# Kernel tuning notes

Measured on AMD Instinct MI355X. Metric: run time of the kernel, lower is better.

## Reference

```python
import jax, jax.numpy as jnp
import numpy as np

COST_CLASS, COST_MASK, COST_DICE = 2.0, 5.0, 5.0
NUM_POINTS = 12544

def setup_inputs() -> dict:
    key = jax.random.key(0)
    k1, k2, k3, k4, k5 = jax.random.split(key, 5)
    bs, Q, K = 4, 100, 134
    H = W = 256
    M = 80
    P = H * W
    pred_logits = jax.random.normal(k1, (bs, Q, K), dtype=jnp.float32)
    pred_masks = jax.random.normal(k2, (bs, Q, H, W), dtype=jnp.float32)
    tgt_labels = jax.random.randint(k3, (M,), 0, K - 1, dtype=jnp.int32)
    # binary target masks, stored as float (matches .float() in torch code)
    tgt_masks = (jax.random.uniform(k4, (M, H, W)) > 0.5).astype(jnp.float32)
    # random subset of points without replacement (torch.randperm[:num_points])
    point_idx = jax.random.permutation(k5, P)[:NUM_POINTS].astype(jnp.int32)
    return {"pred_logits": pred_logits, "pred_masks": pred_masks,
            "tgt_labels": tgt_labels, "tgt_masks": tgt_masks,
            "point_idx": point_idx}

def reference(pred_logits, pred_masks, tgt_labels, tgt_masks, point_idx):
    bs, Q, K = pred_logits.shape
    N = bs * Q
    M = tgt_masks.shape[0]
    Pn = point_idx.shape[0]

    # class cost: -p[n, tgt_id[m]]
    out_prob = jax.nn.softmax(pred_logits.reshape(N, K), axis=-1)
    tgt_ids = jnp.clip(tgt_labels.astype(jnp.int32), 0, K - 1)
    cost_class = -out_prob[:, tgt_ids]                      # (N, M)

    # sampled mask logits / targets
    x = pred_masks.reshape(N, -1)[:, point_idx]             # (N, Pn) logits
    y = tgt_masks.reshape(M, -1)[:, point_idx]              # (M, Pn) binary float

    # BCE-with-logits cost, separable form:
    # mean_p[softplus(x) - x*y] = mean_p softplus(x) - (x @ y^T)/Pn
    sp_mean = jnp.mean(jax.nn.softplus(x), axis=-1)         # (N,)
    xy = jnp.einsum('np,mp->nm', x, y)                      # (N, M)
    cost_mask = sp_mean[:, None] - xy / Pn

    # dice cost
    s = jax.nn.sigmoid(x)                                   # (N, Pn)
    numer = 2.0 * jnp.einsum('np,mp->nm', s, y)             # (N, M)
    denom = jnp.sum(s, axis=-1)[:, None] + jnp.sum(y, axis=-1)[None, :]
    cost_dice = 1.0 - (numer + 1.0) / (denom + 1.0)

    C = COST_CLASS * cost_class + COST_MASK * cost_mask + COST_DICE * cost_dice
    return C.reshape(bs, Q, M)
```

## Files before the change

kernel.cpp:

```cpp
#include <hip/hip_runtime.h>
#include <math.h>

#define N_ROWS 400
#define M_ROWS 80
#define K_CLS  134
#define PN     12544
#define PFULL  65536
#define WORDS  (PFULL / 32)
#define NSUB   25
#define TSTEPS 392
#define TPB    2
#define KCG    49

#define GY_BLOCKS 245

#define CROWS  (N_ROWS + M_ROWS)
#define CHUNK  16384
#define CPB    (PFULL / CHUNK)

typedef __attribute__((ext_vector_type(4))) float  f32x4;
typedef __attribute__((ext_vector_type(8))) __bf16 bf16x8;

__device__ __forceinline__ float wave_reduce_sum(float v) {
#pragma unroll
    for (int off = 32; off > 0; off >>= 1) v += __shfl_down(v, off, 64);
    return v;
}

__global__ __launch_bounds__(1024) void sort_softmax_kernel(
        const int* __restrict__ point_idx,
        unsigned int* __restrict__ bitmap_g, int* __restrict__ rank_g,
        const float* __restrict__ pred_logits,
        float* __restrict__ rowmax, float* __restrict__ rowsum) {
    int tid = threadIdx.x;
    if (blockIdx.x == 0) {
        __shared__ unsigned int bits[WORDS];
        __shared__ int wtot[16], wbase[16];
        bits[tid] = 0u; bits[tid + 1024] = 0u;
        __syncthreads();
        for (int i = tid; i < PN; i += 1024) {
            int p = point_idx[i];
            atomicOr(&bits[p >> 5], 1u << (p & 31));
        }
        __syncthreads();
        unsigned int w0 = bits[tid * 2], w1 = bits[tid * 2 + 1];
        int cnt = __popc(w0) + __popc(w1);
        int lane = tid & 63, wid = tid >> 6;
        int v = cnt;
#pragma unroll
        for (int off = 1; off < 64; off <<= 1) {
            int u = __shfl_up(v, off, 64);
            if (lane >= off) v += u;
        }
        if (lane == 63) wtot[wid] = v;
        __syncthreads();
        if (tid == 0) {
            int run = 0;
#pragma unroll
            for (int i = 0; i < 16; ++i) { wbase[i] = run; run += wtot[i]; }
        }
        __syncthreads();
        int base = wbase[wid] + (v - cnt);
        bitmap_g[tid * 2]     = w0;
        bitmap_g[tid * 2 + 1] = w1;
        rank_g[tid * 2]       = base;
        rank_g[tid * 2 + 1]   = base + __popc(w0);
    } else {
        int wave = tid >> 6, lane = tid & 63;
        int n = (blockIdx.x - 1) * 16 + wave;
        const float* row = pred_logits + n * K_CLS;
        float mx = -1e30f;
        for (int k = lane; k < K_CLS; k += 64) mx = fmaxf(mx, row[k]);
#pragma unroll
        for (int off = 32; off > 0; off >>= 1) mx = fmaxf(mx, __shfl_down(mx, off, 64));
        mx = __shfl(mx, 0, 64);
        float se = 0.f;
        for (int k = lane; k < K_CLS; k += 64) se += expf(row[k] - mx);
        se = wave_reduce_sum(se);
        if (lane == 0) { rowmax[n] = mx; rowsum[n] = se; }
    }
}

__global__ __launch_bounds__(256) void compact_kernel(
        const float* __restrict__ pred_masks, const float* __restrict__ tgt_masks,
        const unsigned int* __restrict__ bitmap_g, const int* __restrict__ rank_g,
        float* __restrict__ Xc, float* __restrict__ Yc) {
    __shared__ unsigned int sb[CHUNK / 32];
    __shared__ int swb[CHUNK / 32];
    int b   = blockIdx.x;
    int row = b / CPB, ch = b % CPB;
    int tid = threadIdx.x;
    int w0  = ch * (CHUNK / 32);
    sb[tid]        = bitmap_g[w0 + tid];
    sb[tid + 256]  = bitmap_g[w0 + tid + 256];
    swb[tid]       = rank_g[w0 + tid];
    swb[tid + 256] = rank_g[w0 + tid + 256];
    __syncthreads();

    const float* src; float* dst;
    if (row < N_ROWS) {
        src = pred_masks + (size_t)row * PFULL;
        dst = Xc + (size_t)row * PN;
    } else {
        src = tgt_masks + (size_t)(row - N_ROWS) * PFULL;
        dst = Yc + (size_t)(row - N_ROWS) * PN;
    }
    int p0 = ch * CHUNK;
#pragma unroll
    for (int it = 0; it < CHUNK / (256 * 4); ++it) {
        int e = (it * 256 + tid) * 4;
        f32x4 v = *(const f32x4*)(src + p0 + e);
        unsigned int w = sb[e >> 5];
        int r = swb[e >> 5] + __popc(w & ((1u << (e & 31)) - 1u));
        unsigned int m4 = (w >> (e & 31)) & 0xFu;
        if (m4 & 1u) { dst[r++] = v[0]; }
        if (m4 & 2u) { dst[r++] = v[1]; }
        if (m4 & 4u) { dst[r++] = v[2]; }
        if (m4 & 8u) { dst[r]   = v[3]; }
    }
}

__global__ __launch_bounds__(512) void gather_y_kernel(
        const float* __restrict__ Yc,
        __bf16* __restrict__ Yb, float* __restrict__ ypart) {
    __shared__ float smem[128];
    int b = blockIdx.x;
    int j = b / 49, tch = b % 49;
    int wave = threadIdx.x >> 6, lane = threadIdx.x & 63;
    int colL = lane & 15, quad = lane >> 4;
    int m = 16 * j + colL;
    int t = tch * 8 + wave;
    int k0 = t * 32 + quad * 8;
    const float* yrow = Yc + (size_t)m * PN;
    f32x4 a = *(const f32x4*)(yrow + k0);
    f32x4 c = *(const f32x4*)(yrow + k0 + 4);
    bf16x8 v; float acc = 0.f;
#pragma unroll
    for (int jj = 0; jj < 4; ++jj) {
        v[jj]     = (__bf16)a[jj]; acc += a[jj];
        v[jj + 4] = (__bf16)c[jj]; acc += c[jj];
    }
    ((bf16x8*)Yb)[(size_t)(t * 5 + j) * 64 + lane] = v;
    acc += __shfl_down(acc, 32, 64);
    acc += __shfl_down(acc, 16, 64);
    if (quad == 0) smem[wave * 16 + colL] = acc;
    __syncthreads();
    if (threadIdx.x < 16) {
        float s = 0.f;
#pragma unroll
        for (int wv = 0; wv < 8; ++wv) s += smem[wv * 16 + threadIdx.x];
        ypart[tch * M_ROWS + 16 * j + threadIdx.x] = s;
    }
}

__global__ __launch_bounds__(256) void gemm_fused_kernel(
        const float* __restrict__ Xc,
        const __bf16* __restrict__ Yb,
        float* __restrict__ xypart, float* __restrict__ sypart,
        float* __restrict__ rowS, float* __restrict__ rowSP) {
    __shared__ float red[4][40][64];
    __shared__ float rowred[4][2][16];
    int wave = threadIdx.x >> 6, lane = threadIdx.x & 63;
    int nsub = blockIdx.x / KCG, kcg = blockIdx.x % KCG;
    int kc = kcg * 4 + wave;
    int n0 = nsub * 16;
    int colL = lane & 15, quad = lane >> 4;
    int tbase = kc * TPB;

    const float* row = Xc + (size_t)(n0 + colL) * PN;
    const bf16x8* Yfrag = (const bf16x8*)Yb;

    f32x4 accX[5], accS[5];
    f32x4 zero = {0.f, 0.f, 0.f, 0.f};
#pragma unroll
    for (int j = 0; j < 5; ++j) { accX[j] = zero; accS[j] = zero; }
    float sumS = 0.f, sumSP = 0.f;

    float xs[TPB][8];
    bf16x8 Bbuf[TPB][5];
#pragma unroll
    for (int i = 0; i < TPB; ++i) {
        int t = tbase + i;
        int k0 = t * 32 + quad * 8;
        f32x4 a = *(const f32x4*)(row + k0);
        f32x4 c = *(const f32x4*)(row + k0 + 4);
#pragma unroll
        for (int jj = 0; jj < 4; ++jj) { xs[i][jj] = a[jj]; xs[i][jj + 4] = c[jj]; }
        const bf16x8* q = Yfrag + (size_t)(t * 5) * 64 + lane;
#pragma unroll
        for (int j = 0; j < 5; ++j) Bbuf[i][j] = q[(size_t)j * 64];
    }
#pragma unroll
    for (int i = 0; i < TPB; ++i) {
        bf16x8 aX, aS;
#pragma unroll
        for (int jj = 0; jj < 8; ++jj) {
            float x  = xs[i][jj];
            float ax = fabsf(x);
            float e  = __expf(-ax);
            float inv = __builtin_amdgcn_rcpf(1.f + e);
            float sig = (x >= 0.f) ? inv : e * inv;
            float sp  = fmaxf(x, 0.f) + __logf(1.f + e);
            aX[jj] = (__bf16)x; aS[jj] = (__bf16)sig;
            sumS += sig; sumSP += sp;
        }
#pragma unroll
        for (int j = 0; j < 5; ++j) {
            accX[j] = __builtin_amdgcn_mfma_f32_16x16x32_bf16(aX, Bbuf[i][j], accX[j], 0, 0, 0);
            accS[j] = __builtin_amdgcn_mfma_f32_16x16x32_bf16(aS, Bbuf[i][j], accS[j], 0, 0, 0);
        }
    }

#pragma unroll
    for (int j = 0; j < 5; ++j)
#pragma unroll
        for (int r = 0; r < 4; ++r) {
            red[wave][j * 4 + r][lane]      = accX[j][r];
            red[wave][20 + j * 4 + r][lane] = accS[j][r];
        }
    sumS  += __shfl_down(sumS, 32, 64);
    sumS  += __shfl_down(sumS, 16, 64);
    sumSP += __shfl_down(sumSP, 32, 64);
    sumSP += __shfl_down(sumSP, 16, 64);
    if (lane < 16) { rowred[wave][0][lane] = sumS; rowred[wave][1][lane] = sumSP; }
    __syncthreads();
#pragma unroll
    for (int v0 = 0; v0 < 10; ++v0) {
        int v = wave * 10 + v0;
        float s = red[0][v][lane] + red[1][v][lane] + red[2][v][lane] + red[3][v][lane];
        int vv = (v < 20) ? v : v - 20;
        int j = vv >> 2, r = vv & 3;
        int n = n0 + quad * 4 + r, m = 16 * j + colL;
        float* dst = (v < 20) ? xypart : sypart;
        dst[(size_t)kcg * (N_ROWS * M_ROWS) + n * M_ROWS + m] = s;
    }
    if (threadIdx.x < 16) {
        rowS[kcg * N_ROWS + n0 + threadIdx.x] =
            rowred[0][0][threadIdx.x] + rowred[1][0][threadIdx.x] +
            rowred[2][0][threadIdx.x] + rowred[3][0][threadIdx.x];
    } else if (threadIdx.x < 32) {
        int l = threadIdx.x - 16;
        rowSP[kcg * N_ROWS + n0 + l] =
            rowred[0][1][l] + rowred[1][1][l] + rowred[2][1][l] + rowred[3][1][l];
    }
}

__global__ void combine_kernel(const float* __restrict__ logits,
                               const int* __restrict__ tgt_labels,
                               const float* __restrict__ rowmax,
                               const float* __restrict__ rowsum,
                               const float* __restrict__ rowS,
                               const float* __restrict__ rowSP,
                               const float* __restrict__ ypart,
                               const float* __restrict__ xypart,
                               const float* __restrict__ sypart,
                               float* __restrict__ out) {
    int idx = blockIdx.x * blockDim.x + threadIdx.x;
    if (idx >= N_ROWS * M_ROWS) return;
    int n = idx / M_ROWS, m = idx % M_ROWS;
    float xy = 0.f, sy = 0.f, ssumv = 0.f, spsumv = 0.f, ysum = 0.f;
#pragma unroll 7
    for (int g = 0; g < KCG; ++g) {
        xy += xypart[(size_t)g * (N_ROWS * M_ROWS) + idx];
        sy += sypart[(size_t)g * (N_ROWS * M_ROWS) + idx];
        ssumv  += rowS[g * N_ROWS + n];
        spsumv += rowSP[g * N_ROWS + n];
        ysum += ypart[g * M_ROWS + m];
    }
    int tid = tgt_labels[m];
    tid = min(max(tid, 0), K_CLS - 1);
    float p = expf(logits[n * K_CLS + tid] - rowmax[n]) / rowsum[n];
    float cost_class = -p;
    float cost_mask = (spsumv - xy) * (1.0f / PN);
    float cost_dice = 1.f - (2.f * sy + 1.f) / (ssumv + ysum + 1.f);
    out[idx] = 2.f * cost_class + 5.f * cost_mask + 5.f * cost_dice;
}

extern "C" void kernel_launch(void* const* d_in, const int* in_sizes, int n_in,
                              void* d_out, int out_size, void* d_ws, size_t ws_size,
                              hipStream_t stream) {
    const float* pred_logits = (const float*)d_in[0];
    const float* pred_masks  = (const float*)d_in[1];
    const int*   tgt_labels  = (const int*)d_in[2];
    const float* tgt_masks   = (const float*)d_in[3];
    const int*   point_idx   = (const int*)d_in[4];
    float* out = (float*)d_out;

    char* ws = (char*)d_ws;
    size_t off = 0;
    auto carve = [&](size_t nbytes) {
        char* p = ws + off;
        off += (nbytes + 255) & ~(size_t)255;
        return p;
    };
    unsigned int* bitmap = (unsigned int*)carve(WORDS * 4);
    int*   rankp  = (int*)carve(WORDS * 4);
    float* rowmax = (float*)carve(N_ROWS * 4);
    float* rowsum = (float*)carve(N_ROWS * 4);
    float* ypart  = (float*)carve(KCG * M_ROWS * 4);
    float* rowS   = (float*)carve(KCG * N_ROWS * 4);
    float* rowSP  = (float*)carve(KCG * N_ROWS * 4);
    float* xypart = (float*)carve((size_t)KCG * N_ROWS * M_ROWS * 4);
    float* sypart = (float*)carve((size_t)KCG * N_ROWS * M_ROWS * 4);
    __bf16* Yb = (__bf16*)carve((size_t)TSTEPS * 5 * 1024);
    float* Xc = (float*)carve((size_t)N_ROWS * PN * 4);
    float* Yc = (float*)carve((size_t)M_ROWS * PN * 4);
    (void)ws_size; (void)in_sizes; (void)n_in; (void)out_size;

    sort_softmax_kernel<<<26, 1024, 0, stream>>>(point_idx, bitmap, rankp,
                                                 pred_logits, rowmax, rowsum);
    compact_kernel<<<CROWS * CPB, 256, 0, stream>>>(pred_masks, tgt_masks,
                                                    bitmap, rankp, Xc, Yc);
    gather_y_kernel<<<GY_BLOCKS, 512, 0, stream>>>(Yc, Yb, ypart);
    gemm_fused_kernel<<<NSUB * KCG, 256, 0, stream>>>(
        Xc, Yb, xypart, sypart, rowS, rowSP);
    combine_kernel<<<(N_ROWS * M_ROWS + 255) / 256, 256, 0, stream>>>(
        pred_logits, tgt_labels, rowmax, rowsum, rowS, rowSP, ypart, xypart, sypart, out);
}
```

Measured before the change: 223.0 us.

## Fuse sigmoid/softplus and bf16 packing into compaction, drop gather_y kernel

```diff
diff --git a/kernel.cpp b/kernel.cpp
--- a/kernel.cpp
+++ b/kernel.cpp
@@ -7,14 +7,11 @@
 #define PN     12544
 #define PFULL  65536
 #define WORDS  (PFULL / 32)
+#define TSTEPS 392
 #define NSUB   25
-#define TSTEPS 392
+#define KCG    49
 #define TPB    2
-#define KCG    49
-
-#define GY_BLOCKS 245
-
-#define CROWS  (N_ROWS + M_ROWS)
+#define NM     (N_ROWS * M_ROWS)
 #define CHUNK  16384
 #define CPB    (PFULL / CHUNK)
 
@@ -30,6 +27,8 @@
 __global__ __launch_bounds__(1024) void sort_softmax_kernel(
         const int* __restrict__ point_idx,
         unsigned int* __restrict__ bitmap_g, int* __restrict__ rank_g,
+        float* __restrict__ rowS_acc, float* __restrict__ rowSP_acc,
+        float* __restrict__ ysum_acc,
         const float* __restrict__ pred_logits,
         float* __restrict__ rowmax, float* __restrict__ rowsum) {
     int tid = threadIdx.x;
@@ -37,6 +36,8 @@
         __shared__ unsigned int bits[WORDS];
         __shared__ int wtot[16], wbase[16];
         bits[tid] = 0u; bits[tid + 1024] = 0u;
+        if (tid < N_ROWS) { rowS_acc[tid] = 0.f; rowSP_acc[tid] = 0.f; }
+        if (tid < M_ROWS) ysum_acc[tid] = 0.f;
         __syncthreads();
         for (int i = tid; i < PN; i += 1024) {
             int p = point_idx[i];
@@ -84,196 +85,193 @@
 __global__ __launch_bounds__(256) void compact_kernel(
         const float* __restrict__ pred_masks, const float* __restrict__ tgt_masks,
         const unsigned int* __restrict__ bitmap_g, const int* __restrict__ rank_g,
-        float* __restrict__ Xc, float* __restrict__ Yc) {
+        __bf16* __restrict__ Xc, __bf16* __restrict__ Sc, __bf16* __restrict__ Yb,
+        float* __restrict__ rowS_acc, float* __restrict__ rowSP_acc,
+        float* __restrict__ ysum_acc) {
     __shared__ unsigned int sb[CHUNK / 32];
     __shared__ int swb[CHUNK / 32];
+    __shared__ float aS[4], aSP[4];
     int b   = blockIdx.x;
     int row = b / CPB, ch = b % CPB;
     int tid = threadIdx.x;
+    int wave = tid >> 6, lane = tid & 63;
     int w0  = ch * (CHUNK / 32);
     sb[tid]        = bitmap_g[w0 + tid];
     sb[tid + 256]  = bitmap_g[w0 + tid + 256];
     swb[tid]       = rank_g[w0 + tid];
     swb[tid + 256] = rank_g[w0 + tid + 256];
     __syncthreads();
-
-    const float* src; float* dst;
+    int p0 = ch * CHUNK;
+
     if (row < N_ROWS) {
-        src = pred_masks + (size_t)row * PFULL;
-        dst = Xc + (size_t)row * PN;
+        const float* src = pred_masks + (size_t)row * PFULL + p0;
+        __bf16* xrow = Xc + (size_t)row * PN;
+        __bf16* srow = Sc + (size_t)row * PN;
+        float sS = 0.f, sSP = 0.f;
+#pragma unroll
+        for (int it = 0; it < CHUNK / (256 * 4); ++it) {
+            int e = (it * 256 + tid) * 4;
+            f32x4 v = *(const f32x4*)(src + e);
+            unsigned int w = sb[e >> 5];
+            int r = swb[e >> 5] + __popc(w & ((1u << (e & 31)) - 1u));
+            unsigned int m4 = (w >> (e & 31)) & 0xFu;
+            if (m4) {
+#pragma unroll
+                for (int k = 0; k < 4; ++k) if (m4 & (1u << k)) {
+                    float x  = v[k];
+                    float ax = fabsf(x);
+                    float ee = __expf(-ax);
+                    float den = 1.f + ee;
+                    float inv = __builtin_amdgcn_rcpf(den);
+                    float sig = (x >= 0.f) ? inv : ee * inv;
+                    float sp  = fmaxf(x, 0.f) + __logf(den);
+                    xrow[r] = (__bf16)x;
+                    srow[r] = (__bf16)sig;
+                    sS += sig; sSP += sp; ++r;
+                }
+            }
+        }
+        sS  = wave_reduce_sum(sS);
+        sSP = wave_reduce_sum(sSP);
+        if (lane == 0) { aS[wave] = sS; aSP[wave] = sSP; }
+        __syncthreads();
+        if (tid == 0)
+            atomicAdd(&rowS_acc[row], aS[0] + aS[1] + aS[2] + aS[3]);
+        else if (tid == 1)
+            atomicAdd(&rowSP_acc[row], aSP[0] + aSP[1] + aSP[2] + aSP[3]);
     } else {
-        src = tgt_masks + (size_t)(row - N_ROWS) * PFULL;
-        dst = Yc + (size_t)(row - N_ROWS) * PN;
-    }
-    int p0 = ch * CHUNK;
-#pragma unroll
-    for (int it = 0; it < CHUNK / (256 * 4); ++it) {
-        int e = (it * 256 + tid) * 4;
-        f32x4 v = *(const f32x4*)(src + p0 + e);
-        unsigned int w = sb[e >> 5];
-        int r = swb[e >> 5] + __popc(w & ((1u << (e & 31)) - 1u));
-        unsigned int m4 = (w >> (e & 31)) & 0xFu;
-        if (m4 & 1u) { dst[r++] = v[0]; }
-        if (m4 & 2u) { dst[r++] = v[1]; }
-        if (m4 & 4u) { dst[r++] = v[2]; }
-        if (m4 & 8u) { dst[r]   = v[3]; }
-    }
-}
-
-__global__ __launch_bounds__(512) void gather_y_kernel(
-        const float* __restrict__ Yc,
-        __bf16* __restrict__ Yb, float* __restrict__ ypart) {
-    __shared__ float smem[128];
-    int b = blockIdx.x;
-    int j = b / 49, tch = b % 49;
-    int wave = threadIdx.x >> 6, lane = threadIdx.x & 63;
+        int m = row - N_ROWS;
+        const float* src = tgt_masks + (size_t)m * PFULL + p0;
+        int j = m >> 4, colL = m & 15;
+        float ys = 0.f;
+#pragma unroll
+        for (int it = 0; it < CHUNK / (256 * 4); ++it) {
+            int e = (it * 256 + tid) * 4;
+            f32x4 v = *(const f32x4*)(src + e);
+            unsigned int w = sb[e >> 5];
+            int r = swb[e >> 5] + __popc(w & ((1u << (e & 31)) - 1u));
+            unsigned int m4 = (w >> (e & 31)) & 0xFu;
+            if (m4) {
+#pragma unroll
+                for (int k = 0; k < 4; ++k) if (m4 & (1u << k)) {
+                    float y = (v[k] > 0.5f) ? 1.f : 0.f;
+                    int t = r >> 5, rr = r & 31;
+                    int quad = rr >> 3, jj = rr & 7;
+                    Yb[(((size_t)t * 5 + j) * 64 + quad * 16 + colL) * 8 + jj]
+                        = (__bf16)y;
+                    ys += y; ++r;
+                }
+            }
+        }
+        ys = wave_reduce_sum(ys);
+        if (lane == 0) aS[wave] = ys;
+        __syncthreads();
+        if (tid == 0)
+            atomicAdd(&ysum_acc[m], aS[0] + aS[1] + aS[2] + aS[3]);
+    }
+}
+
+__global__ __launch_bounds__(256) void gemm_kernel(
+        const __bf16* __restrict__ Xc, const __bf16* __restrict__ Sc,
+        const __bf16* __restrict__ Yb,
+        float* __restrict__ xypart, float* __restrict__ sypart) {
+    __shared__ float red[4][20][64];
+    int tid = threadIdx.x;
+    int wave = tid >> 6, lane = tid & 63;
     int colL = lane & 15, quad = lane >> 4;
-    int m = 16 * j + colL;
-    int t = tch * 8 + wave;
-    int k0 = t * 32 + quad * 8;
-    const float* yrow = Yc + (size_t)m * PN;
-    f32x4 a = *(const f32x4*)(yrow + k0);
-    f32x4 c = *(const f32x4*)(yrow + k0 + 4);
-    bf16x8 v; float acc = 0.f;
-#pragma unroll
-    for (int jj = 0; jj < 4; ++jj) {
-        v[jj]     = (__bf16)a[jj]; acc += a[jj];
-        v[jj + 4] = (__bf16)c[jj]; acc += c[jj];
-    }
-    ((bf16x8*)Yb)[(size_t)(t * 5 + j) * 64 + lane] = v;
-    acc += __shfl_down(acc, 32, 64);
-    acc += __shfl_down(acc, 16, 64);
-    if (quad == 0) smem[wave * 16 + colL] = acc;
-    __syncthreads();
-    if (threadIdx.x < 16) {
-        float s = 0.f;
-#pragma unroll
-        for (int wv = 0; wv < 8; ++wv) s += smem[wv * 16 + threadIdx.x];
-        ypart[tch * M_ROWS + 16 * j + threadIdx.x] = s;
-    }
-}
-
-__global__ __launch_bounds__(256) void gemm_fused_kernel(
-        const float* __restrict__ Xc,
-        const __bf16* __restrict__ Yb,
-        float* __restrict__ xypart, float* __restrict__ sypart,
-        float* __restrict__ rowS, float* __restrict__ rowSP) {
-    __shared__ float red[4][40][64];
-    __shared__ float rowred[4][2][16];
-    int wave = threadIdx.x >> 6, lane = threadIdx.x & 63;
-    int nsub = blockIdx.x / KCG, kcg = blockIdx.x % KCG;
-    int kc = kcg * 4 + wave;
+    int nsub = blockIdx.x % NSUB, kcg = blockIdx.x / NSUB;
     int n0 = nsub * 16;
-    int colL = lane & 15, quad = lane >> 4;
-    int tbase = kc * TPB;
-
-    const float* row = Xc + (size_t)(n0 + colL) * PN;
-    const bf16x8* Yfrag = (const bf16x8*)Yb;
+    int tbase = kcg * (TPB * 4) + wave * TPB;
+    const bf16x8* Yf = (const bf16x8*)Yb;
 
     f32x4 accX[5], accS[5];
     f32x4 zero = {0.f, 0.f, 0.f, 0.f};
 #pragma unroll
     for (int j = 0; j < 5; ++j) { accX[j] = zero; accS[j] = zero; }
-    float sumS = 0.f, sumSP = 0.f;
-
-    float xs[TPB][8];
-    bf16x8 Bbuf[TPB][5];
+
+    bf16x8 aX[TPB], aS[TPB], Bb[TPB][5];
 #pragma unroll
     for (int i = 0; i < TPB; ++i) {
         int t = tbase + i;
-        int k0 = t * 32 + quad * 8;
-        f32x4 a = *(const f32x4*)(row + k0);
-        f32x4 c = *(const f32x4*)(row + k0 + 4);
-#pragma unroll
-        for (int jj = 0; jj < 4; ++jj) { xs[i][jj] = a[jj]; xs[i][jj + 4] = c[jj]; }
-        const bf16x8* q = Yfrag + (size_t)(t * 5) * 64 + lane;
-#pragma unroll
-        for (int j = 0; j < 5; ++j) Bbuf[i][j] = q[(size_t)j * 64];
+        size_t aoff = (size_t)(n0 + colL) * PN + t * 32 + quad * 8;
+        aX[i] = *(const bf16x8*)(Xc + aoff);
+        aS[i] = *(const bf16x8*)(Sc + aoff);
+        const bf16x8* q = Yf + (size_t)(t * 5) * 64 + lane;
+#pragma unroll
+        for (int j = 0; j < 5; ++j) Bb[i][j] = q[(size_t)j * 64];
     }
 #pragma unroll
     for (int i = 0; i < TPB; ++i) {
-        bf16x8 aX, aS;
-#pragma unroll
-        for (int jj = 0; jj < 8; ++jj) {
-            float x  = xs[i][jj];
-            float ax = fabsf(x);
-            float e  = __expf(-ax);
-            float inv = __builtin_amdgcn_rcpf(1.f + e);
-            float sig = (x >= 0.f) ? inv : e * inv;
-            float sp  = fmaxf(x, 0.f) + __logf(1.f + e);
-            aX[jj] = (__bf16)x; aS[jj] = (__bf16)sig;
-            sumS += sig; sumSP += sp;
-        }
 #pragma unroll
         for (int j = 0; j < 5; ++j) {
-            accX[j] = __builtin_amdgcn_mfma_f32_16x16x32_bf16(aX, Bbuf[i][j], accX[j], 0, 0, 0);
-            accS[j] = __builtin_amdgcn_mfma_f32_16x16x32_bf16(aS, Bbuf[i][j], accS[j], 0, 0, 0);
+            accX[j] = __builtin_amdgcn_mfma_f32_16x16x32_bf16(aX[i], Bb[i][j], accX[j], 0, 0, 0);
+            accS[j] = __builtin_amdgcn_mfma_f32_16x16x32_bf16(aS[i], Bb[i][j], accS[j], 0, 0, 0);
         }
     }
 
 #pragma unroll
     for (int j = 0; j < 5; ++j)
 #pragma unroll
-        for (int r = 0; r < 4; ++r) {
-            red[wave][j * 4 + r][lane]      = accX[j][r];
-            red[wave][20 + j * 4 + r][lane] = accS[j][r];
-        }
-    sumS  += __shfl_down(sumS, 32, 64);
-    sumS  += __shfl_down(sumS, 16, 64);
-    sumSP += __shfl_down(sumSP, 32, 64);
-    sumSP += __shfl_down(sumSP, 16, 64);
-    if (lane < 16) { rowred[wave][0][lane] = sumS; rowred[wave][1][lane] = sumSP; }
-    __syncthreads();
-#pragma unroll
-    for (int v0 = 0; v0 < 10; ++v0) {
-        int v = wave * 10 + v0;
+        for (int r = 0; r < 4; ++r) red[wave][j * 4 + r][lane] = accX[j][r];
+    __syncthreads();
+#pragma unroll
+    for (int v0 = 0; v0 < 5; ++v0) {
+        int v = wave * 5 + v0;
         float s = red[0][v][lane] + red[1][v][lane] + red[2][v][lane] + red[3][v][lane];
-        int vv = (v < 20) ? v : v - 20;
-        int j = vv >> 2, r = vv & 3;
+        int j = v >> 2, r = v & 3;
         int n = n0 + quad * 4 + r, m = 16 * j + colL;
-        float* dst = (v < 20) ? xypart : sypart;
-        dst[(size_t)kcg * (N_ROWS * M_ROWS) + n * M_ROWS + m] = s;
-    }
-    if (threadIdx.x < 16) {
-        rowS[kcg * N_ROWS + n0 + threadIdx.x] =
-            rowred[0][0][threadIdx.x] + rowred[1][0][threadIdx.x] +
-            rowred[2][0][threadIdx.x] + rowred[3][0][threadIdx.x];
-    } else if (threadIdx.x < 32) {
-        int l = threadIdx.x - 16;
-        rowSP[kcg * N_ROWS + n0 + l] =
-            rowred[0][1][l] + rowred[1][1][l] + rowred[2][1][l] + rowred[3][1][l];
-    }
-}
-
-__global__ void combine_kernel(const float* __restrict__ logits,
-                               const int* __restrict__ tgt_labels,
-                               const float* __restrict__ rowmax,
-                               const float* __restrict__ rowsum,
-                               const float* __restrict__ rowS,
-                               const float* __restrict__ rowSP,
-                               const float* __restrict__ ypart,
-                               const float* __restrict__ xypart,
-                               const float* __restrict__ sypart,
-                               float* __restrict__ out) {
-    int idx = blockIdx.x * blockDim.x + threadIdx.x;
-    if (idx >= N_ROWS * M_ROWS) return;
+        xypart[(size_t)kcg * NM + n * M_ROWS + m] = s;
+    }
+    __syncthreads();
+#pragma unroll
+    for (int j = 0; j < 5; ++j)
+#pragma unroll
+        for (int r = 0; r < 4; ++r) red[wave][j * 4 + r][lane] = accS[j][r];
+    __syncthreads();
+#pragma unroll
+    for (int v0 = 0; v0 < 5; ++v0) {
+        int v = wave * 5 + v0;
+        float s = red[0][v][lane] + red[1][v][lane] + red[2][v][lane] + red[3][v][lane];
+        int j = v >> 2, r = v & 3;
+        int n = n0 + quad * 4 + r, m = 16 * j + colL;
+        sypart[(size_t)kcg * NM + n * M_ROWS + m] = s;
+    }
+}
+
+__global__ __launch_bounds__(256) void combine_kernel(
+        const float* __restrict__ logits,
+        const int* __restrict__ tgt_labels,
+        const float* __restrict__ rowmax,
+        const float* __restrict__ rowsum,
+        const float* __restrict__ rowS_acc,
+        const float* __restrict__ rowSP_acc,
+        const float* __restrict__ ysum_acc,
+        const float* __restrict__ xypart,
+        const float* __restrict__ sypart,
+        float* __restrict__ out) {
+    __shared__ float sxy[4][64], ssy[4][64];
+    int il = threadIdx.x & 63, q = threadIdx.x >> 6;
+    int idx = blockIdx.x * 64 + il;
     int n = idx / M_ROWS, m = idx % M_ROWS;
-    float xy = 0.f, sy = 0.f, ssumv = 0.f, spsumv = 0.f, ysum = 0.f;
-#pragma unroll 7
-    for (int g = 0; g < KCG; ++g) {
-        xy += xypart[(size_t)g * (N_ROWS * M_ROWS) + idx];
-        sy += sypart[(size_t)g * (N_ROWS * M_ROWS) + idx];
-        ssumv  += rowS[g * N_ROWS + n];
-        spsumv += rowSP[g * N_ROWS + n];
-        ysum += ypart[g * M_ROWS + m];
-    }
-    int tid = tgt_labels[m];
-    tid = min(max(tid, 0), K_CLS - 1);
-    float p = expf(logits[n * K_CLS + tid] - rowmax[n]) / rowsum[n];
-    float cost_class = -p;
-    float cost_mask = (spsumv - xy) * (1.0f / PN);
-    float cost_dice = 1.f - (2.f * sy + 1.f) / (ssumv + ysum + 1.f);
-    out[idx] = 2.f * cost_class + 5.f * cost_mask + 5.f * cost_dice;
+    float xy = 0.f, sy = 0.f;
+    for (int g = q; g < KCG; g += 4) {
+        xy += xypart[(size_t)g * NM + idx];
+        sy += sypart[(size_t)g * NM + idx];
+    }
+    sxy[q][il] = xy; ssy[q][il] = sy;
+    __syncthreads();
+    if (q == 0) {
+        xy = sxy[0][il] + sxy[1][il] + sxy[2][il] + sxy[3][il];
+        sy = ssy[0][il] + ssy[1][il] + ssy[2][il] + ssy[3][il];
+        float ss = rowS_acc[n], sp = rowSP_acc[n], ysum = ysum_acc[m];
+        int tc = tgt_labels[m];
+        tc = min(max(tc, 0), K_CLS - 1);
+        float p = expf(logits[n * K_CLS + tc] - rowmax[n]) / rowsum[n];
+        float cost_class = -p;
+        float cost_mask = (sp - xy) * (1.0f / PN);
+        float cost_dice = 1.f - (2.f * sy + 1.f) / (ss + ysum + 1.f);
+        out[idx] = 2.f * cost_class + 5.f * cost_mask + 5.f * cost_dice;
+    }
 }
 
 extern "C" void kernel_launch(void* const* d_in, const int* in_sizes, int n_in,
@@ -297,23 +295,24 @@
     int*   rankp  = (int*)carve(WORDS * 4);
     float* rowmax = (float*)carve(N_ROWS * 4);
     float* rowsum = (float*)carve(N_ROWS * 4);
-    float* ypart  = (float*)carve(KCG * M_ROWS * 4);
-    float* rowS   = (float*)carve(KCG * N_ROWS * 4);
-    float* rowSP  = (float*)carve(KCG * N_ROWS * 4);
-    float* xypart = (float*)carve((size_t)KCG * N_ROWS * M_ROWS * 4);
-    float* sypart = (float*)carve((size_t)KCG * N_ROWS * M_ROWS * 4);
+    float* rowS_acc  = (float*)carve(N_ROWS * 4);
+    float* rowSP_acc = (float*)carve(N_ROWS * 4);
+    float* ysum_acc  = (float*)carve(M_ROWS * 4);
+    __bf16* Xc = (__bf16*)carve((size_t)N_ROWS * PN * 2);
+    __bf16* Sc = (__bf16*)carve((size_t)N_ROWS * PN * 2);
     __bf16* Yb = (__bf16*)carve((size_t)TSTEPS * 5 * 1024);
-    float* Xc = (float*)carve((size_t)N_ROWS * PN * 4);
-    float* Yc = (float*)carve((size_t)M_ROWS * PN * 4);
+    float* xypart = (float*)carve((size_t)KCG * NM * 4);
+    float* sypart = (float*)carve((size_t)KCG * NM * 4);
     (void)ws_size; (void)in_sizes; (void)n_in; (void)out_size;
 
-    sort_softmax_kernel<<<26, 1024, 0, stream>>>(point_idx, bitmap, rankp,
-                                                 pred_logits, rowmax, rowsum);
-    compact_kernel<<<CROWS * CPB, 256, 0, stream>>>(pred_masks, tgt_masks,
-                                                    bitmap, rankp, Xc, Yc);
-    gather_y_kernel<<<GY_BLOCKS, 512, 0, stream>>>(Yc, Yb, ypart);
-    gemm_fused_kernel<<<NSUB * KCG, 256, 0, stream>>>(
-        Xc, Yb, xypart, sypart, rowS, rowSP);
-    combine_kernel<<<(N_ROWS * M_ROWS + 255) / 256, 256, 0, stream>>>(
-        pred_logits, tgt_labels, rowmax, rowsum, rowS, rowSP, ypart, xypart, sypart, out);
-}
+    sort_softmax_kernel<<<26, 1024, 0, stream>>>(
+        point_idx, bitmap, rankp, rowS_acc, rowSP_acc, ysum_acc,
+        pred_logits, rowmax, rowsum);
+    compact_kernel<<<(N_ROWS + M_ROWS) * CPB, 256, 0, stream>>>(
+        pred_masks, tgt_masks, bitmap, rankp, Xc, Sc, Yb,
+        rowS_acc, rowSP_acc, ysum_acc);
+    gemm_kernel<<<NSUB * KCG, 256, 0, stream>>>(Xc, Sc, Yb, xypart, sypart);
+    combine_kernel<<<NM / 64, 256, 0, stream>>>(
+        pred_logits, tgt_labels, rowmax, rowsum, rowS_acc, rowSP_acc,
+        ysum_acc, xypart, sypart, out);
+}
```

Result: faster. 215.3 us (-3.5%).
